# Optimization experiments

Hardware: AMD Instinct MI355X
Metric: run time of the kernel (lower is better)

The kernel has to match this reference:

```python
import jax, jax.numpy as jnp
import numpy as np

N_NODES = 100000


def _gcn_conv(x, src, dst, W, b, n_nodes):
    # PyG GCNConv: out = D^{-1/2} (A + I) D^{-1/2} (x W) + b
    h = x @ W  # [N, out]
    # degree including self-loop
    ones = jnp.ones(src.shape[0], dtype=h.dtype)
    deg = jax.ops.segment_sum(ones, dst, num_segments=n_nodes) + 1.0
    dinv = jax.lax.rsqrt(deg)  # [N]
    # neighbor messages: gather from src, normalize, scatter-add to dst
    norm = dinv[src] * dinv[dst]  # [E]
    msg = h[src] * norm[:, None]  # [E, out]
    agg = jax.ops.segment_sum(msg, dst, num_segments=n_nodes)
    # self-loop contribution: norm_ii = dinv[i]^2
    agg = agg + h * (dinv * dinv)[:, None]
    return agg + b


def setup_inputs() -> dict:
    key = jax.random.key(0)
    ks = jax.random.split(key, 10)
    x = jax.random.normal(ks[0], (N_NODES, 64), dtype=jnp.float32)
    edge_index = jax.random.randint(ks[1], (2, 1000000), 0, N_NODES, dtype=jnp.int64)
    def glorot(k, shape):
        lim = np.sqrt(6.0 / (shape[0] + shape[1]))
        return jax.random.uniform(k, shape, jnp.float32, -lim, lim)
    return {
        "x": x,
        "edge_index": edge_index,
        "W1": glorot(ks[2], (64, 80)), "b1": jnp.zeros((80,), jnp.float32),
        "W2": glorot(ks[3], (80, 40)), "b2": jnp.zeros((40,), jnp.float32),
        "W3": glorot(ks[4], (40, 50)), "b3": jnp.zeros((50,), jnp.float32),
        "Wl": glorot(ks[5], (50, 10)), "bl": jnp.zeros((10,), jnp.float32),
    }


def reference(x, edge_index, W1, b1, W2, b2, W3, b3, Wl, bl):
    src, dst = edge_index[0], edge_index[1]
    n = x.shape[0]
    h = _gcn_conv(x, src, dst, W1, b1, n)
    h = jax.nn.leaky_relu(h, negative_slope=0.01)
    # dropout is identity in eval mode
    h = _gcn_conv(h, src, dst, W2, b2, n)
    h = jax.nn.leaky_relu(h, negative_slope=0.01)
    h = _gcn_conv(h, src, dst, W3, b3, n)
    h = jax.nn.leaky_relu(h, negative_slope=0.01)
    logits = h @ Wl + bl
    return jax.nn.log_softmax(logits, axis=1)
```

## Files before the change

### kernel.cpp

```cpp
#include <hip/hip_runtime.h>

#define LEAKY(v) ((v) > 0.0f ? (v) : 0.01f * (v))
#define NBUK_MAX 512

typedef __attribute__((ext_vector_type(8))) short bf16x8;
typedef __attribute__((ext_vector_type(4))) float f32x4;

__device__ __forceinline__ unsigned short f2bf(float f) {
    unsigned u = __float_as_uint(f);
    u += 0x7fffu + ((u >> 16) & 1u);
    return (unsigned short)(u >> 16);
}
__device__ __forceinline__ unsigned pack2bf(float lo, float hi) {
    return (unsigned)f2bf(lo) | ((unsigned)f2bf(hi) << 16);
}
__device__ __forceinline__ float4 bf4_to_f4(uint2 u) {
    float4 r;
    r.x = __uint_as_float(u.x << 16);
    r.y = __uint_as_float(u.x & 0xffff0000u);
    r.z = __uint_as_float(u.y << 16);
    r.w = __uint_as_float(u.y & 0xffff0000u);
    return r;
}

__device__ __forceinline__ int detect_is64(const unsigned* ei, int E) {
    __shared__ int is64_s;
    if (threadIdx.x == 0) {
        int z = 1;
        int limit = 2 * E < 128 ? 2 * E : 128;
        for (int i = 1; i < limit; i += 2)
            if (ei[i] != 0u) { z = 0; break; }
        is64_s = z;
    }
    __syncthreads();
    return is64_s;
}

__global__ __launch_bounds__(256) void bucket_count_kernel(
    const unsigned* __restrict__ ei, int* __restrict__ s32, int* __restrict__ d32,
    int* __restrict__ gcount, int E, int nblk, int nbuk, int ch) {
    __shared__ int hist[NBUK_MAX];
    int is64 = detect_is64(ei, E);
    for (int i = threadIdx.x; i < nbuk; i += 256) hist[i] = 0;
    __syncthreads();
    int base = blockIdx.x * ch;
    int lim = min(base + ch, E);
    for (int e = base + threadIdx.x; e < lim; e += 256) {
        int s, d;
        if (is64) {
            s = (int)ei[2 * (size_t)e];
            d = (int)ei[2 * (size_t)E + 2 * (size_t)e];
        } else {
            s = (int)ei[e];
            d = (int)ei[(size_t)E + e];
        }
        s32[e] = s;
        d32[e] = d;
        atomicAdd(&hist[d >> 8], 1);
    }
    __syncthreads();
    for (int i = threadIdx.x; i < nbuk; i += 256)
        gcount[(size_t)i * nblk + blockIdx.x] = hist[i];
}

__global__ __launch_bounds__(256) void bucket_total_kernel(
    const int* __restrict__ gcount, int* __restrict__ btot, int nblk) {
    __shared__ int s[256];
    int sum = 0;
    for (int i = threadIdx.x; i < nblk; i += 256)
        sum += gcount[(size_t)blockIdx.x * nblk + i];
    s[threadIdx.x] = sum;
    __syncthreads();
    for (int off = 128; off > 0; off >>= 1) {
        if (threadIdx.x < off) s[threadIdx.x] += s[threadIdx.x + off];
        __syncthreads();
    }
    if (threadIdx.x == 0) btot[blockIdx.x] = s[0];
}

__global__ __launch_bounds__(512) void scan_btot_kernel(
    const int* __restrict__ btot, int* __restrict__ bbase,
    int* __restrict__ row_ofs, int nbuk, int N, int E) {
    __shared__ int s[512];
    int t = threadIdx.x;
    int v = (t < nbuk) ? btot[t] : 0;
    s[t] = v;
    __syncthreads();
    for (int off = 1; off < 512; off <<= 1) {
        int add = (t >= off) ? s[t - off] : 0;
        __syncthreads();
        s[t] += add;
        __syncthreads();
    }
    if (t < nbuk) bbase[t] = s[t] - v;
    if (t == 0) { bbase[nbuk] = E; row_ofs[N] = E; }
}

__global__ __launch_bounds__(256) void scan_gcount_kernel(
    int* __restrict__ gcount, const int* __restrict__ bbase, int nblk) {
    __shared__ int s[256];
    int t = threadIdx.x;
    int v = (t < nblk) ? gcount[(size_t)blockIdx.x * nblk + t] : 0;
    s[t] = v;
    __syncthreads();
    for (int off = 1; off < 256; off <<= 1) {
        int add = (t >= off) ? s[t - off] : 0;
        __syncthreads();
        s[t] += add;
        __syncthreads();
    }
    if (t < nblk)
        gcount[(size_t)blockIdx.x * nblk + t] = bbase[blockIdx.x] + s[t] - v;
}

__global__ __launch_bounds__(256) void bucket_scatter_kernel(
    const int* __restrict__ s32, const int* __restrict__ d32,
    const int* __restrict__ gofs, unsigned* __restrict__ es_tmp,
    int E, int nblk, int nbuk, int ch) {
    __shared__ int cur[NBUK_MAX];
    for (int i = threadIdx.x; i < nbuk; i += 256)
        cur[i] = gofs[(size_t)i * nblk + blockIdx.x];
    __syncthreads();
    int base = blockIdx.x * ch;
    int lim = min(base + ch, E);
    for (int e = base + threadIdx.x; e < lim; e += 256) {
        int s = s32[e], d = d32[e];
        int p = atomicAdd(&cur[d >> 8], 1);
        es_tmp[p] = ((unsigned)(d & 255) << 24) | (unsigned)s;
    }
}

__global__ __launch_bounds__(256) void bucket_sortcvt_kernel(
    const unsigned* __restrict__ es_tmp, const int* __restrict__ bbase,
    int* __restrict__ es, int* __restrict__ row_ofs, float* __restrict__ dinv,
    const float* __restrict__ x, ushort4* __restrict__ xb, int N) {
    __shared__ int hist[256];
    __shared__ int lofs[256];
    __shared__ float sdinv[256];
    int b = blockIdx.x;
    int t = threadIdx.x;
    int beg = bbase[b], end = bbase[b + 1];
    hist[t] = 0;
    __syncthreads();
    for (int j = beg + t; j < end; j += 256)
        atomicAdd(&hist[es_tmp[j] >> 24], 1);
    __syncthreads();
    int v = hist[t];
    lofs[t] = v;
    __syncthreads();
    for (int off = 1; off < 256; off <<= 1) {
        int add = (t >= off) ? lofs[t - off] : 0;
        __syncthreads();
        lofs[t] += add;
        __syncthreads();
    }
    int excl = lofs[t] - v;
    int node = (b << 8) + t;
    float dv = rsqrtf((float)v + 1.0f);
    if (node <= N) row_ofs[node] = beg + excl;
    if (node < N) dinv[node] = dv;
    sdinv[t] = dv;
    __syncthreads();
    lofs[t] = beg + excl;
    __syncthreads();
    for (int j = beg + t; j < end; j += 256) {
        unsigned ed = es_tmp[j];
        int p = atomicAdd(&lofs[ed >> 24], 1);
        es[p] = (int)(ed & 0xFFFFFFu);
    }
    int qbase = (b << 8) * 16;
    for (int q = t; q < 256 * 16; q += 256) {
        int nl = q >> 4;
        int n = (b << 8) + nl;
        if (n >= N) break;
        float dn = sdinv[nl];
        float4 vv = ((const float4*)x)[qbase + q];
        ushort4 o;
        o.x = f2bf(vv.x * dn); o.y = f2bf(vv.y * dn);
        o.z = f2bf(vv.z * dn); o.w = f2bf(vv.w * dn);
        xb[qbase + q] = o;
    }
}

__global__ __launch_bounds__(256) void prep_wfrags_kernel(
    const float* __restrict__ W1, const float* __restrict__ W2,
    unsigned short* __restrict__ wfrag) {
    int t = blockIdx.x * 256 + threadIdx.x;
    if (t >= 2432) return;
    const float* W;
    int u, NKC, M, K;
    if (t < 1280) { u = t; W = W1; NKC = 2; M = 80; K = 64; }
    else          { u = t - 1280; W = W2; NKC = 3; M = 40; K = 80; }
    int f = u >> 6, lane = u & 63;
    int s = f & 1, mtkc = f >> 1;
    int kc = mtkc % NKC, mt = mtkc / NKC;
    int col = mt * 16 + (lane & 15);
#pragma unroll
    for (int j = 0; j < 8; ++j) {
        int k = kc * 32 + ((lane >> 4) << 3) + j;
        float w = (k < K && col < M) ? W[k * M + col] : 0.0f;
        unsigned short hi = f2bf(w);
        unsigned short v = s ? f2bf(w - __uint_as_float((unsigned)hi << 16)) : hi;
        wfrag[(size_t)t * 8 + j] = v;
    }
}

__global__ __launch_bounds__(256) void l1_fused_kernel(
    const unsigned short* __restrict__ xb, const int* __restrict__ es,
    const int* __restrict__ row_ofs, const float* __restrict__ dinv,
    const unsigned short* __restrict__ wfrag, const float* __restrict__ b1,
    unsigned short* __restrict__ out, int N) {
    constexpr int NFR = 20;
    __shared__ bf16x8 wlds[NFR * 64];
    for (int i = threadIdx.x; i < NFR * 64; i += 256) {
        int f = i >> 6, ln = i & 63;
        wlds[f * 64 + (ln ^ (ln >> 3))] = *(const bf16x8*)&wfrag[(size_t)i * 8];
    }
    __syncthreads();
    int wid = blockIdx.x * 4 + (threadIdx.x >> 6);
    int ntiles = (N + 15) >> 4;
    if (wid >= ntiles) return;
    int lane = threadIdx.x & 63;
    int row = lane & 15, kid = lane >> 4;
    int lidx = lane ^ (lane >> 3);
    int base = wid * 16;
    int node = base + row;
    bool act = node < N;
    int beg = 0, end = 0;
    float dd = 0.f;
    if (act) {
        beg = row_ofs[node];
        end = row_ofs[node + 1];
        dd = dinv[node];
    }
    const char* xbb = (const char*)xb;
    const int o0 = kid * 16;
    const int o1 = 64 + kid * 16;
    float4 aL0 = make_float4(0.f, 0.f, 0.f, 0.f);
    float4 aL1 = make_float4(0.f, 0.f, 0.f, 0.f);
    float4 aH0 = make_float4(0.f, 0.f, 0.f, 0.f);
    float4 aH1 = make_float4(0.f, 0.f, 0.f, 0.f);
#define ACCU(u, c0, c1)                                             \
    {                                                               \
        float4 lo_ = bf4_to_f4(make_uint2((u).x, (u).y));           \
        float4 hi_ = bf4_to_f4(make_uint2((u).z, (u).w));           \
        c0.x += lo_.x; c0.y += lo_.y; c0.z += lo_.z; c0.w += lo_.w; \
        c1.x += hi_.x; c1.y += hi_.y; c1.z += hi_.z; c1.w += hi_.w; \
    }
    int j = beg;
    for (; j + 4 <= end; j += 4) {
        int s0 = es[j], s1 = es[j + 1], s2 = es[j + 2], s3 = es[j + 3];
        const char* p0 = xbb + (size_t)s0 * 128;
        const char* p1 = xbb + (size_t)s1 * 128;
        const char* p2 = xbb + (size_t)s2 * 128;
        const char* p3 = xbb + (size_t)s3 * 128;
        uint4 u00 = *(const uint4*)(p0 + o0);
        uint4 u01 = *(const uint4*)(p0 + o1);
        uint4 u10 = *(const uint4*)(p1 + o0);
        uint4 u11 = *(const uint4*)(p1 + o1);
        uint4 u20 = *(const uint4*)(p2 + o0);
        uint4 u21 = *(const uint4*)(p2 + o1);
        uint4 u30 = *(const uint4*)(p3 + o0);
        uint4 u31 = *(const uint4*)(p3 + o1);
        ACCU(u00, aL0, aL1) ACCU(u01, aH0, aH1)
        ACCU(u10, aL0, aL1) ACCU(u11, aH0, aH1)
        ACCU(u20, aL0, aL1) ACCU(u21, aH0, aH1)
        ACCU(u30, aL0, aL1) ACCU(u31, aH0, aH1)
    }
    for (; j < end; ++j) {
        int s0 = es[j];
        const char* p0 = xbb + (size_t)s0 * 128;
        uint4 u00 = *(const uint4*)(p0 + o0);
        uint4 u01 = *(const uint4*)(p0 + o1);
        ACCU(u00, aL0, aL1) ACCU(u01, aH0, aH1)
    }
    if (act) {
        const char* ps = xbb + (size_t)node * 128;
        uint4 us0 = *(const uint4*)(ps + o0);
        uint4 us1 = *(const uint4*)(ps + o1);
        ACCU(us0, aL0, aL1) ACCU(us1, aH0, aH1)
    }
#undef ACCU
    bf16x8 a0, a1;
    a0[0] = (short)f2bf(aL0.x * dd); a0[1] = (short)f2bf(aL0.y * dd);
    a0[2] = (short)f2bf(aL0.z * dd); a0[3] = (short)f2bf(aL0.w * dd);
    a0[4] = (short)f2bf(aL1.x * dd); a0[5] = (short)f2bf(aL1.y * dd);
    a0[6] = (short)f2bf(aL1.z * dd); a0[7] = (short)f2bf(aL1.w * dd);
    a1[0] = (short)f2bf(aH0.x * dd); a1[1] = (short)f2bf(aH0.y * dd);
    a1[2] = (short)f2bf(aH0.z * dd); a1[3] = (short)f2bf(aH0.w * dd);
    a1[4] = (short)f2bf(aH1.x * dd); a1[5] = (short)f2bf(aH1.y * dd);
    a1[6] = (short)f2bf(aH1.z * dd); a1[7] = (short)f2bf(aH1.w * dd);

    f32x4 acc[5];
#pragma unroll
    for (int mt = 0; mt < 5; ++mt) acc[mt] = (f32x4){0.f, 0.f, 0.f, 0.f};
#pragma unroll
    for (int mt = 0; mt < 5; ++mt) {
        acc[mt] = __builtin_amdgcn_mfma_f32_16x16x32_bf16(
            a0, wlds[((mt * 2 + 0) * 2 + 0) * 64 + lidx], acc[mt], 0, 0, 0);
        acc[mt] = __builtin_amdgcn_mfma_f32_16x16x32_bf16(
            a0, wlds[((mt * 2 + 0) * 2 + 1) * 64 + lidx], acc[mt], 0, 0, 0);
        acc[mt] = __builtin_amdgcn_mfma_f32_16x16x32_bf16(
            a1, wlds[((mt * 2 + 1) * 2 + 0) * 64 + lidx], acc[mt], 0, 0, 0);
        acc[mt] = __builtin_amdgcn_mfma_f32_16x16x32_bf16(
            a1, wlds[((mt * 2 + 1) * 2 + 1) * 64 + lidx], acc[mt], 0, 0, 0);
    }
#pragma unroll
    for (int mt = 0; mt < 5; ++mt) {
        int col = mt * 16 + (lane & 15);
        float bb = b1[col];
#pragma unroll
        for (int r = 0; r < 4; ++r) {
            int orow = base + kid * 4 + r;
            if (orow < N) {
                float v = acc[mt][r] + bb;
                v = LEAKY(v);
                out[(size_t)orow * 80 + col] = f2bf(v);
            }
        }
    }
}

template <bool BIAS, bool PRESCALE_LEAKY>
__global__ __launch_bounds__(256) void gather40_bf16_kernel(
    const unsigned short* __restrict__ hb, const int* __restrict__ es,
    const int* __restrict__ row_ofs, const float* __restrict__ dinv,
    const float* __restrict__ b, unsigned short* __restrict__ agg, int N) {
    int wid = (blockIdx.x * blockDim.x + threadIdx.x) >> 6;
    int lane = threadIdx.x & 63;
    int g = lane / 5;
    int l = lane - g * 5;
    int node = wid * 12 + g;
    bool active = (g < 12) && (node < N);
    int beg = 0, end = 0;
    float dd = 0.f;
    if (active) {
        beg = row_ofs[node];
        end = row_ofs[node + 1];
        dd = dinv[node];
    }
    float4 aL = make_float4(0.f, 0.f, 0.f, 0.f);
    float4 aH = make_float4(0.f, 0.f, 0.f, 0.f);
#define ACC40(u)                                                    \
    {                                                               \
        float4 lo_ = bf4_to_f4(make_uint2((u).x, (u).y));           \
        float4 hi_ = bf4_to_f4(make_uint2((u).z, (u).w));           \
        aL.x += lo_.x; aL.y += lo_.y; aL.z += lo_.z; aL.w += lo_.w; \
        aH.x += hi_.x; aH.y += hi_.y; aH.z += hi_.z; aH.w += hi_.w; \
    }
    int j = beg;
    for (; j + 4 <= end; j += 4) {
        int s0 = es[j], s1 = es[j + 1], s2 = es[j + 2], s3 = es[j + 3];
        uint4 h0 = *(const uint4*)&hb[(size_t)s0 * 40 + 8 * l];
        uint4 h1 = *(const uint4*)&hb[(size_t)s1 * 40 + 8 * l];
        uint4 h2 = *(const uint4*)&hb[(size_t)s2 * 40 + 8 * l];
        uint4 h3 = *(const uint4*)&hb[(size_t)s3 * 40 + 8 * l];
        ACC40(h0) ACC40(h1) ACC40(h2) ACC40(h3)
    }
    for (; j < end; ++j) {
        int s0 = es[j];
        uint4 h0 = *(const uint4*)&hb[(size_t)s0 * 40 + 8 * l];
        ACC40(h0)
    }
#undef ACC40
    if (active) {
        uint4 sr = *(const uint4*)&hb[(size_t)node * 40 + 8 * l];
        float4 sL = bf4_to_f4(make_uint2(sr.x, sr.y));
        float4 sH = bf4_to_f4(make_uint2(sr.z, sr.w));
        float r0 = (aL.x + sL.x) * dd, r1 = (aL.y + sL.y) * dd;
        float r2 = (aL.z + sL.z) * dd, r3 = (aL.w + sL.w) * dd;
        float r4 = (aH.x + sH.x) * dd, r5 = (aH.y + sH.y) * dd;
        float r6 = (aH.z + sH.z) * dd, r7 = (aH.w + sH.w) * dd;
        if (BIAS) {
            float4 b0 = *(const float4*)&b[8 * l];
            float4 b1 = *(const float4*)&b[8 * l + 4];
            r0 += b0.x; r1 += b0.y; r2 += b0.z; r3 += b0.w;
            r4 += b1.x; r5 += b1.y; r6 += b1.z; r7 += b1.w;
        }
        if (PRESCALE_LEAKY) {
            r0 = LEAKY(r0) * dd; r1 = LEAKY(r1) * dd;
            r2 = LEAKY(r2) * dd; r3 = LEAKY(r3) * dd;
            r4 = LEAKY(r4) * dd; r5 = LEAKY(r5) * dd;
            r6 = LEAKY(r6) * dd; r7 = LEAKY(r7) * dd;
        }
        uint4 o;
        o.x = pack2bf(r0, r1); o.y = pack2bf(r2, r3);
        o.z = pack2bf(r4, r5); o.w = pack2bf(r6, r7);
        *(uint4*)&agg[(size_t)node * 40 + 8 * l] = o;
    }
}

template <int KBF, int M, int NKC, int NMT, bool LEAKY_OUT, bool BIAS, bool SCALE>
__global__ __launch_bounds__(256) void gemm_mfma_bf16(
    const unsigned short* __restrict__ X, const unsigned short* __restrict__ wfrag,
    const float* __restrict__ bvec, const float* __restrict__ dinv,
    unsigned short* __restrict__ out, int N) {
    static_assert(KBF <= NKC * 32 && M <= NMT * 16, "tile coverage");
    constexpr int NFR = NMT * NKC * 2;
    __shared__ bf16x8 wlds[NFR * 64];
    for (int i = threadIdx.x; i < NFR * 64; i += 256) {
        int f = i >> 6, ln = i & 63;
        wlds[f * 64 + (ln ^ (ln >> 3))] = *(const bf16x8*)&wfrag[(size_t)i * 8];
    }
    __syncthreads();
    int wid = blockIdx.x * 4 + (threadIdx.x >> 6);
    int ntiles = (N + 15) >> 4;
    if (wid >= ntiles) return;
    int lane = threadIdx.x & 63;
    int kid = lane >> 4;
    int lidx = lane ^ (lane >> 3);
    int base = wid * 16;
    int arow = base + (lane & 15);
    if (arow >= N) arow = N - 1;

    bf16x8 a[NKC];
#pragma unroll
    for (int kc = 0; kc < NKC; ++kc) {
        int k0 = kc * 32 + kid * 8;
        if (k0 < KBF)
            a[kc] = *(const bf16x8*)&X[(size_t)arow * KBF + k0];
        else
            a[kc] = (bf16x8){0, 0, 0, 0, 0, 0, 0, 0};
    }
    f32x4 acc[NMT];
#pragma unroll
    for (int mt = 0; mt < NMT; ++mt) acc[mt] = (f32x4){0.f, 0.f, 0.f, 0.f};
#pragma unroll
    for (int mt = 0; mt < NMT; ++mt) {
#pragma unroll
        for (int kc = 0; kc < NKC; ++kc) {
            acc[mt] = __builtin_amdgcn_mfma_f32_16x16x32_bf16(
                a[kc], wlds[((mt * NKC + kc) * 2 + 0) * 64 + lidx], acc[mt], 0, 0, 0);
            acc[mt] = __builtin_amdgcn_mfma_f32_16x16x32_bf16(
                a[kc], wlds[((mt * NKC + kc) * 2 + 1) * 64 + lidx], acc[mt], 0, 0, 0);
        }
    }
    float dv[4];
#pragma unroll
    for (int r = 0; r < 4; ++r)
        dv[r] = SCALE ? dinv[min(base + kid * 4 + r, N - 1)] : 1.0f;
#pragma unroll
    for (int mt = 0; mt < NMT; ++mt) {
        int col = mt * 16 + (lane & 15);
        if (col >= M) continue;
        float bb = BIAS ? bvec[col] : 0.0f;
#pragma unroll
        for (int r = 0; r < 4; ++r) {
            int orow = base + kid * 4 + r;
            if (orow < N) {
                float v = acc[mt][r] + bb;
                if (LEAKY_OUT) v = LEAKY(v);
                if (SCALE) v *= dv[r];
                out[(size_t)orow * M + col] = f2bf(v);
            }
        }
    }
}

__global__ __launch_bounds__(256) void l3head_kernel(
    const unsigned short* __restrict__ P, const float* __restrict__ W3,
    const float* __restrict__ b3, const float* __restrict__ Wl,
    const float* __restrict__ bl, float* __restrict__ out, int N) {
    __shared__ float w3s[40 * 50];
    __shared__ float b3s[50];
    __shared__ float wls[50 * 10];
    __shared__ float bls[10];
    for (int i = threadIdx.x; i < 2000; i += 256) w3s[i] = W3[i];
    for (int i = threadIdx.x; i < 500; i += 256) wls[i] = Wl[i];
    if (threadIdx.x < 50) b3s[threadIdx.x] = b3[threadIdx.x];
    if (threadIdx.x < 10) bls[threadIdx.x] = bl[threadIdx.x];
    __syncthreads();
    int n = blockIdx.x * blockDim.x + threadIdx.x;
    if (n >= N) return;

    float p[40];
    const uint2* pr = (const uint2*)(P + (size_t)n * 40);
#pragma unroll
    for (int q = 0; q < 10; ++q) {
        float4 t = bf4_to_f4(pr[q]);
        p[4 * q + 0] = t.x; p[4 * q + 1] = t.y; p[4 * q + 2] = t.z; p[4 * q + 3] = t.w;
    }
    float logits[10];
#pragma unroll
    for (int j = 0; j < 10; ++j) logits[j] = bls[j];
    for (int m = 0; m < 50; ++m) {
        float acc = b3s[m];
#pragma unroll
        for (int k = 0; k < 40; ++k) acc = fmaf(p[k], w3s[k * 50 + m], acc);
        float v = LEAKY(acc);
#pragma unroll
        for (int j = 0; j < 10; ++j) logits[j] = fmaf(v, wls[m * 10 + j], logits[j]);
    }
    float mx = logits[0];
#pragma unroll
    for (int j = 1; j < 10; ++j) mx = fmaxf(mx, logits[j]);
    float s = 0.0f;
#pragma unroll
    for (int j = 0; j < 10; ++j) s += __expf(logits[j] - mx);
    float lse = __logf(s) + mx;
    float* op = out + (size_t)n * 10;
#pragma unroll
    for (int j = 0; j < 10; ++j) op[j] = logits[j] - lse;
}

extern "C" void kernel_launch(void* const* d_in, const int* in_sizes, int n_in,
                              void* d_out, int out_size, void* d_ws, size_t ws_size,
                              hipStream_t stream) {
    const float* x  = (const float*)d_in[0];
    const unsigned* ei = (const unsigned*)d_in[1];
    const float* W1 = (const float*)d_in[2];
    const float* b1 = (const float*)d_in[3];
    const float* W2 = (const float*)d_in[4];
    const float* b2 = (const float*)d_in[5];
    const float* W3 = (const float*)d_in[6];
    const float* b3 = (const float*)d_in[7];
    const float* Wl = (const float*)d_in[8];
    const float* bl = (const float*)d_in[9];
    float* out = (float*)d_out;

    const int N = in_sizes[0] / 64;
    const int E = in_sizes[1] / 2;

    int ch = 4096;
    int nblk = (E + ch - 1) / ch;
    if (nblk > 256) { ch = (E + 255) / 256; nblk = (E + ch - 1) / ch; }
    const int nbuk = (N + 255) >> 8;

    char* wp = (char*)d_ws;
    auto alloc = [&](size_t bytes) {
        char* p = wp;
        wp += (bytes + 255) & ~(size_t)255;
        return p;
    };
    int*   es      = (int*)alloc((size_t)E * 4);
    float* dinv    = (float*)alloc((size_t)N * 4);
    int*   row_ofs = (int*)alloc((size_t)(N + 1) * 4);
    int*   gcount  = (int*)alloc((size_t)nbuk * nblk * 4);
    int*   btot    = (int*)alloc((size_t)NBUK_MAX * 4);
    int*   bbase   = (int*)alloc((size_t)(NBUK_MAX + 1) * 4);
    unsigned short* wfrag = (unsigned short*)alloc((size_t)2432 * 8 * 2);
    char*  Pr      = (char*)alloc((size_t)N * 64 * 4);
    char*  Ar      = (char*)alloc((size_t)N * 80 * 4);

    int*      s32    = (int*)Pr;
    int*      d32    = (int*)Pr + E;
    unsigned* es_tmp = (unsigned*)Ar;
    size_t xb_off = (((size_t)E * 4) + 255) & ~(size_t)255;
    unsigned short* xb = (unsigned short*)(Ar + xb_off);
    unsigned short* A  = (unsigned short*)Pr;
    unsigned short* Pb = (unsigned short*)Ar;
    unsigned short* Ab = (unsigned short*)(Ar + (size_t)N * 80 * 4 - (size_t)N * 40 * 2);
    unsigned short* P3 = (unsigned short*)Pr;

    const int B = 256;

    prep_wfrags_kernel<<<10, B, 0, stream>>>(W1, W2, wfrag);

    bucket_count_kernel<<<nblk, B, 0, stream>>>(ei, s32, d32, gcount, E, nblk, nbuk, ch);
    bucket_total_kernel<<<nbuk, B, 0, stream>>>(gcount, btot, nblk);
    scan_btot_kernel<<<1, 512, 0, stream>>>(btot, bbase, row_ofs, nbuk, N, E);
    scan_gcount_kernel<<<nbuk, B, 0, stream>>>(gcount, bbase, nblk);
    bucket_scatter_kernel<<<nblk, B, 0, stream>>>(s32, d32, gcount, es_tmp, E, nblk, nbuk, ch);
    bucket_sortcvt_kernel<<<nbuk, B, 0, stream>>>(es_tmp, bbase, es, row_ofs, dinv,
                                                  x, (ushort4*)xb, N);

    const int blk40 = ((N + 11) / 12 + 3) / 4;
    const int ntiles = (N + 15) / 16;
    const int gemm_blocks = (ntiles + 3) / 4;

    l1_fused_kernel<<<gemm_blocks, B, 0, stream>>>(xb, es, row_ofs, dinv, wfrag, b1, A, N);

    gemm_mfma_bf16<80, 40, 3, 3, false, false, true>
        <<<gemm_blocks, B, 0, stream>>>(A, wfrag + 20 * 512, nullptr, dinv, Pb, N);
    gather40_bf16_kernel<true, true><<<blk40, B, 0, stream>>>(Pb, es, row_ofs, dinv, b2, Ab, N);

    gather40_bf16_kernel<false, false><<<blk40, B, 0, stream>>>(Ab, es, row_ofs, dinv, nullptr, P3, N);
    l3head_kernel<<<(N + B - 1) / B, B, 0, stream>>>(P3, W3, b3, Wl, bl, out, N);
}
```

Measured before the change: 261.0 us.

## Fuse layer-2 GEMM into layer-1 kernel via LDS-staged activation tile

The layer-1 output is no longer written to global memory and re-read by a separate GEMM. Each wave now stages its 16x80 bf16 activation tile in LDS and immediately runs the layer-2 MFMA GEMM against W2 fragments also held in LDS. The kernel writes only the dinv-scaled 40-wide output. This removes one kernel launch and the N×80 bf16 round trip through HBM, at the cost of more LDS per block (38 weight fragments plus four staging tiles), which may reduce occupancy.

```diff
diff --git a/kernel.cpp b/kernel.cpp
--- a/kernel.cpp
+++ b/kernel.cpp
@@ -205,13 +205,14 @@
     }
 }
 
-__global__ __launch_bounds__(256) void l1_fused_kernel(
+__global__ __launch_bounds__(256) void l1l2_fused_kernel(
     const unsigned short* __restrict__ xb, const int* __restrict__ es,
     const int* __restrict__ row_ofs, const float* __restrict__ dinv,
     const unsigned short* __restrict__ wfrag, const float* __restrict__ b1,
-    unsigned short* __restrict__ out, int N) {
-    constexpr int NFR = 20;
+    unsigned short* __restrict__ Pb, int N) {
+    constexpr int NFR = 38;
     __shared__ bf16x8 wlds[NFR * 64];
+    __shared__ unsigned short atile[4][16 * 88];
     for (int i = threadIdx.x; i < NFR * 64; i += 256) {
         int f = i >> 6, ln = i & 63;
         wlds[f * 64 + (ln ^ (ln >> 3))] = *(const bf16x8*)&wfrag[(size_t)i * 8];
@@ -305,18 +306,53 @@
         acc[mt] = __builtin_amdgcn_mfma_f32_16x16x32_bf16(
             a1, wlds[((mt * 2 + 1) * 2 + 1) * 64 + lidx], acc[mt], 0, 0, 0);
     }
+    unsigned short* at = atile[threadIdx.x >> 6];
 #pragma unroll
     for (int mt = 0; mt < 5; ++mt) {
         int col = mt * 16 + (lane & 15);
         float bb = b1[col];
 #pragma unroll
         for (int r = 0; r < 4; ++r) {
+            float v = acc[mt][r] + bb;
+            v = LEAKY(v);
+            at[(kid * 4 + r) * 88 + col] = f2bf(v);
+        }
+    }
+    bf16x8 a2[3];
+#pragma unroll
+    for (int kc = 0; kc < 3; ++kc) {
+        int k0 = kc * 32 + kid * 8;
+        if (k0 + 8 <= 80)
+            a2[kc] = *(const bf16x8*)&at[(lane & 15) * 88 + k0];
+        else
+            a2[kc] = (bf16x8){0, 0, 0, 0, 0, 0, 0, 0};
+    }
+    f32x4 acc2[3];
+#pragma unroll
+    for (int mt = 0; mt < 3; ++mt) acc2[mt] = (f32x4){0.f, 0.f, 0.f, 0.f};
+#pragma unroll
+    for (int mt = 0; mt < 3; ++mt) {
+#pragma unroll
+        for (int kc = 0; kc < 3; ++kc) {
+            acc2[mt] = __builtin_amdgcn_mfma_f32_16x16x32_bf16(
+                a2[kc], wlds[(20 + (mt * 3 + kc) * 2 + 0) * 64 + lidx], acc2[mt], 0, 0, 0);
+            acc2[mt] = __builtin_amdgcn_mfma_f32_16x16x32_bf16(
+                a2[kc], wlds[(20 + (mt * 3 + kc) * 2 + 1) * 64 + lidx], acc2[mt], 0, 0, 0);
+        }
+    }
+    float dvr[4];
+#pragma unroll
+    for (int r = 0; r < 4; ++r)
+        dvr[r] = dinv[min(base + kid * 4 + r, N - 1)];
+#pragma unroll
+    for (int mt = 0; mt < 3; ++mt) {
+        int col = mt * 16 + (lane & 15);
+        if (col >= 40) continue;
+#pragma unroll
+        for (int r = 0; r < 4; ++r) {
             int orow = base + kid * 4 + r;
-            if (orow < N) {
-                float v = acc[mt][r] + bb;
-                v = LEAKY(v);
-                out[(size_t)orow * 80 + col] = f2bf(v);
-            }
+            if (orow < N)
+                Pb[(size_t)orow * 40 + col] = f2bf(acc2[mt][r] * dvr[r]);
         }
     }
 }
@@ -390,73 +426,6 @@
     }
 }
 
-template <int KBF, int M, int NKC, int NMT, bool LEAKY_OUT, bool BIAS, bool SCALE>
-__global__ __launch_bounds__(256) void gemm_mfma_bf16(
-    const unsigned short* __restrict__ X, const unsigned short* __restrict__ wfrag,
-    const float* __restrict__ bvec, const float* __restrict__ dinv,
-    unsigned short* __restrict__ out, int N) {
-    static_assert(KBF <= NKC * 32 && M <= NMT * 16, "tile coverage");
-    constexpr int NFR = NMT * NKC * 2;
-    __shared__ bf16x8 wlds[NFR * 64];
-    for (int i = threadIdx.x; i < NFR * 64; i += 256) {
-        int f = i >> 6, ln = i & 63;
-        wlds[f * 64 + (ln ^ (ln >> 3))] = *(const bf16x8*)&wfrag[(size_t)i * 8];
-    }
-    __syncthreads();
-    int wid = blockIdx.x * 4 + (threadIdx.x >> 6);
-    int ntiles = (N + 15) >> 4;
-    if (wid >= ntiles) return;
-    int lane = threadIdx.x & 63;
-    int kid = lane >> 4;
-    int lidx = lane ^ (lane >> 3);
-    int base = wid * 16;
-    int arow = base + (lane & 15);
-    if (arow >= N) arow = N - 1;
-
-    bf16x8 a[NKC];
-#pragma unroll
-    for (int kc = 0; kc < NKC; ++kc) {
-        int k0 = kc * 32 + kid * 8;
-        if (k0 < KBF)
-            a[kc] = *(const bf16x8*)&X[(size_t)arow * KBF + k0];
-        else
-            a[kc] = (bf16x8){0, 0, 0, 0, 0, 0, 0, 0};
-    }
-    f32x4 acc[NMT];
-#pragma unroll
-    for (int mt = 0; mt < NMT; ++mt) acc[mt] = (f32x4){0.f, 0.f, 0.f, 0.f};
-#pragma unroll
-    for (int mt = 0; mt < NMT; ++mt) {
-#pragma unroll
-        for (int kc = 0; kc < NKC; ++kc) {
-            acc[mt] = __builtin_amdgcn_mfma_f32_16x16x32_bf16(
-                a[kc], wlds[((mt * NKC + kc) * 2 + 0) * 64 + lidx], acc[mt], 0, 0, 0);
-            acc[mt] = __builtin_amdgcn_mfma_f32_16x16x32_bf16(
-                a[kc], wlds[((mt * NKC + kc) * 2 + 1) * 64 + lidx], acc[mt], 0, 0, 0);
-        }
-    }
-    float dv[4];
-#pragma unroll
-    for (int r = 0; r < 4; ++r)
-        dv[r] = SCALE ? dinv[min(base + kid * 4 + r, N - 1)] : 1.0f;
-#pragma unroll
-    for (int mt = 0; mt < NMT; ++mt) {
-        int col = mt * 16 + (lane & 15);
-        if (col >= M) continue;
-        float bb = BIAS ? bvec[col] : 0.0f;
-#pragma unroll
-        for (int r = 0; r < 4; ++r) {
-            int orow = base + kid * 4 + r;
-            if (orow < N) {
-                float v = acc[mt][r] + bb;
-                if (LEAKY_OUT) v = LEAKY(v);
-                if (SCALE) v *= dv[r];
-                out[(size_t)orow * M + col] = f2bf(v);
-            }
-        }
-    }
-}
-
 __global__ __launch_bounds__(256) void l3head_kernel(
     const unsigned short* __restrict__ P, const float* __restrict__ W3,
     const float* __restrict__ b3, const float* __restrict__ Wl,
@@ -547,8 +516,7 @@
     unsigned* es_tmp = (unsigned*)Ar;
     size_t xb_off = (((size_t)E * 4) + 255) & ~(size_t)255;
     unsigned short* xb = (unsigned short*)(Ar + xb_off);
-    unsigned short* A  = (unsigned short*)Pr;
-    unsigned short* Pb = (unsigned short*)Ar;
+    unsigned short* Pb = (unsigned short*)Pr;
     unsigned short* Ab = (unsigned short*)(Ar + (size_t)N * 80 * 4 - (size_t)N * 40 * 2);
     unsigned short* P3 = (unsigned short*)Pr;
 
@@ -568,10 +536,8 @@
     const int ntiles = (N + 15) / 16;
     const int gemm_blocks = (ntiles + 3) / 4;
 
-    l1_fused_kernel<<<gemm_blocks, B, 0, stream>>>(xb, es, row_ofs, dinv, wfrag, b1, A, N);
-
-    gemm_mfma_bf16<80, 40, 3, 3, false, false, true>
-        <<<gemm_blocks, B, 0, stream>>>(A, wfrag + 20 * 512, nullptr, dinv, Pb, N);
+    l1l2_fused_kernel<<<gemm_blocks, B, 0, stream>>>(xb, es, row_ofs, dinv, wfrag, b1, Pb, N);
+
     gather40_bf16_kernel<true, true><<<blk40, B, 0, stream>>>(Pb, es, row_ofs, dinv, b2, Ab, N);
 
     gather40_bf16_kernel<false, false><<<blk40, B, 0, stream>>>(Ab, es, row_ofs, dinv, nullptr, P3, N);
```

After: 257.1 us, median of 2. No clear change (-1.5%).
